# Kernel tuning notes

Hardware: AMD Instinct MI355X
Metric: run time of the kernel (lower is better)

The kernel has to match this reference:

```python
import jax, jax.numpy as jnp
import numpy as np

EPS = 1e-5

def conv1x1(x, w):
    # x: [B,C,T,D,H,W], w: [O,C] -> [B,O,T,D,H,W]
    return jnp.einsum('oc,bctdhw->botdhw', w, x)

def conv4d_3(x, w):
    # 3x3x3x3 4D conv, padding=1, stride=1, decomposed as 3 shifted 3D convs.
    # x: [B,C,T,D,H,W], w: [O,C,3,3,3,3]
    B, C, T, D, H, W = x.shape
    O = w.shape[0]
    xp = jnp.pad(x, ((0, 0), (0, 0), (1, 1), (1, 1), (1, 1), (1, 1)))
    out = None
    for k in range(3):  # small fixed loop over first kernel dim
        xk = xp[:, :, k:k + T]                      # [B,C,T,D+2,H+2,W+2]
        xk = xk.transpose(0, 2, 1, 3, 4, 5).reshape(B * T, C, D + 2, H + 2, W + 2)
        ok = jax.lax.conv_general_dilated(
            xk, w[:, :, k], window_strides=(1, 1, 1), padding='VALID',
            dimension_numbers=('NCDHW', 'OIDHW', 'NCDHW'))  # [B*T,O,D,H,W]
        out = ok if out is None else out + ok
    return out.reshape(B, T, O, D, H, W).transpose(0, 2, 1, 3, 4, 5)

def bn4d(x, g, b):
    # BatchNorm over (B, T, D, H, W) per channel (training-mode batch stats).
    axes = (0, 2, 3, 4, 5)
    m = jnp.mean(x, axis=axes, keepdims=True)
    v = jnp.mean(jnp.square(x - m), axis=axes, keepdims=True)
    sh = (1, -1, 1, 1, 1, 1)
    return (x - m) * jax.lax.rsqrt(v + EPS) * g.reshape(sh) + b.reshape(sh)

def setup_inputs() -> dict:
    key = jax.random.key(0)
    ks = jax.random.split(key, 4)
    B, C, T, D, H, W = 2, 256, 8, 16, 16, 16
    planes = 64
    return {
        'x': jax.random.normal(ks[0], (B, C, T, D, H, W), jnp.float32),
        'w1': jax.random.normal(ks[1], (planes, C), jnp.float32) * 0.05,
        'g1': jnp.ones((planes,), jnp.float32),
        'b1': jnp.zeros((planes,), jnp.float32),
        'w2': jax.random.normal(ks[2], (planes, planes, 3, 3, 3, 3), jnp.float32) * 0.05,
        'g2': jnp.ones((planes,), jnp.float32),
        'b2': jnp.zeros((planes,), jnp.float32),
        'w3': jax.random.normal(ks[3], (4 * planes, planes), jnp.float32) * 0.05,
        'g3': jnp.ones((4 * planes,), jnp.float32),
        'b3': jnp.zeros((4 * planes,), jnp.float32),
    }

def reference(x, w1, g1, b1, w2, g2, b2, w3, g3, b3):
    out = jax.nn.relu(bn4d(conv1x1(x, w1), g1, b1))
    out = jax.nn.relu(bn4d(conv4d_3(out, w2), g2, b2))
    out = bn4d(conv1x1(out, w3), g3, b3)
    return jax.nn.relu(out + x)
```

## Files before the change

### kernel.cpp

```cpp
#include <hip/hip_runtime.h>

#define S_TOT 32768

typedef unsigned short ushortT;
typedef __attribute__((ext_vector_type(8))) short short8;
typedef __attribute__((ext_vector_type(4))) float floatx4;

__device__ __forceinline__ ushortT f2bf(float f) {
    unsigned u = __float_as_uint(f);
    u = (u + 0x7fffu + ((u >> 16) & 1u)) >> 16;
    return (ushortT)u;
}
__device__ __forceinline__ float bf2f(ushortT h) {
    return __uint_as_float(((unsigned)h) << 16);
}
__device__ __forceinline__ uint32_t nrm2(uint32_t u, float a, float bs) {
    float lo = fmaxf(fmaf(a, bf2f((ushortT)(u & 0xffffu)), bs), 0.f);
    float hi = fmaxf(fmaf(a, bf2f((ushortT)(u >> 16)), bs), 0.f);
    return (uint32_t)f2bf(lo) | ((uint32_t)f2bf(hi) << 16);
}

#define NSTRIPE 8
#define STRIDE_ST 768

__global__ __launch_bounds__(256) void k_prep_w(const float* __restrict__ w1,
                                                const float* __restrict__ w2,
                                                const float* __restrict__ w3,
                                                ushortT* __restrict__ wb1,
                                                ushortT* __restrict__ wb2,
                                                ushortT* __restrict__ wb3,
                                                float* __restrict__ stats) {
    int idx = blockIdx.x * 256 + threadIdx.x;
    if (idx < 16384) {
        int e = idx;
        int j = e & 7, o = (e >> 3) & 63, q = (e >> 9) & 3, cc = e >> 11;
        int c = cc * 32 + q * 8 + j;
        wb1[e] = f2bf(w1[o * 256 + c]);
    } else if (idx < 16384 + 331776) {
        int e = idx - 16384;
        int j = e & 7, o = (e >> 3) & 63, cb = (e >> 9) & 7, tap = e >> 12;
        int c = cb * 8 + j;
        wb2[e] = f2bf(w2[((size_t)o * 64 + c) * 81 + tap]);
    } else if (idx < 16384 + 331776 + 16384) {
        int e = idx - 348160;
        int j = e & 7, o = (e >> 3) & 255, g = e >> 11;
        int ks = g >> 2, q = g & 3;
        int c = ks * 32 + q * 8 + j;
        wb3[e] = f2bf(w3[o * 64 + c]);
    } else if (idx < 364544 + NSTRIPE * STRIDE_ST) {
        stats[idx - 364544] = 0.f;
    }
}

__global__ __launch_bounds__(256) void k_conv1_mfma(const float* __restrict__ x,
                                                    const ushortT* __restrict__ wb1,
                                                    ushortT* __restrict__ y1bf,
                                                    float* __restrict__ stats) {
    __shared__ __align__(16) ushortT xb[128 * 40];

    int tid = threadIdx.x;
    int blk = blockIdx.x;
    int b  = blk >> 8;
    int n0 = (blk & 255) * 128;

    int lane = tid & 63;
    int wv   = tid >> 6;
    int m    = lane & 15;
    int q    = lane >> 4;

    int c_loc = tid & 31;
    int ng    = tid >> 5;

    floatx4 acc[8];
#pragma unroll
    for (int i = 0; i < 8; ++i) acc[i] = (floatx4){0.f, 0.f, 0.f, 0.f};

    for (int cc = 0; cc < 8; ++cc) {
        short8 afr = *(const short8*)(wb1 + (((cc * 4 + q) * 64) + wv * 16 + m) * 8);

        __syncthreads();
        {
            int c = cc * 32 + c_loc;
            const float* xp = x + ((size_t)(b * 256 + c)) * S_TOT + n0 + ng * 16;
#pragma unroll
            for (int k = 0; k < 4; ++k) {
                float4 v = *(const float4*)(xp + k * 4);
                int nb = ng * 16 + k * 4;
                xb[(nb + 0) * 40 + c_loc] = f2bf(v.x);
                xb[(nb + 1) * 40 + c_loc] = f2bf(v.y);
                xb[(nb + 2) * 40 + c_loc] = f2bf(v.z);
                xb[(nb + 3) * 40 + c_loc] = f2bf(v.w);
            }
        }
        __syncthreads();

#pragma unroll
        for (int pt = 0; pt < 8; ++pt) {
            short8 bfr = *(const short8*)(xb + (pt * 16 + m) * 40 + q * 8);
            acc[pt] = __builtin_amdgcn_mfma_f32_16x16x32_bf16(afr, bfr, acc[pt], 0, 0, 0);
        }
    }

#pragma unroll
    for (int pt = 0; pt < 8; ++pt) {
#pragma unroll
        for (int r = 0; r < 4; ++r) {
            int o = wv * 16 + q * 4 + r;
            y1bf[((size_t)(b * 64 + o)) * S_TOT + n0 + pt * 16 + m] = f2bf(acc[pt][r]);
        }
    }

    float ssum[4] = {0.f, 0.f, 0.f, 0.f}, ssq[4] = {0.f, 0.f, 0.f, 0.f};
#pragma unroll
    for (int pt = 0; pt < 8; ++pt)
#pragma unroll
        for (int r = 0; r < 4; ++r) {
            float v = acc[pt][r];
            ssum[r] += v;
            ssq[r]  += v * v;
        }
#pragma unroll
    for (int off = 1; off < 16; off <<= 1)
#pragma unroll
        for (int r = 0; r < 4; ++r) {
            ssum[r] += __shfl_xor(ssum[r], off);
            ssq[r]  += __shfl_xor(ssq[r], off);
        }
    if (m == 0) {
        float* st = stats + (blk & (NSTRIPE - 1)) * STRIDE_ST;
#pragma unroll
        for (int r = 0; r < 4; ++r) {
            int o = wv * 16 + q * 4 + r;
            atomicAdd(st + o, ssum[r]);
            atomicAdd(st + 64 + o, ssq[r]);
        }
    }
}

__global__ __launch_bounds__(256, 2) void k_conv2_mfma(
        const ushortT* __restrict__ y1bf,
        const ushortT* __restrict__ wb2,
        const float* __restrict__ g1,
        const float* __restrict__ b1,
        float* __restrict__ stats,
        ushortT* __restrict__ y2bf) {
    __shared__ __align__(16) ushortT xs[180 * 64];
    __shared__ float st2[128];

    int tid = threadIdx.x;
    int blk = blockIdx.x;
    int b  = blk >> 8;
    int t  = (blk >> 5) & 7;
    int d  = (blk >> 1) & 15;
    int h0 = (blk & 1) * 8;

    int lane = tid & 63;
    int wv   = tid >> 6;
    int m    = lane & 15;
    int q    = lane >> 4;
    int wp   = wv & 1;
    int wo   = wv >> 1;

    int c2      = tid & 31;
    int prbase  = tid >> 5;

    if (tid < 128) st2[tid] = 0.f;

    int c0 = 2 * c2, c1v = c0 + 1;
    float s0 = 0.f, q0 = 0.f, s1 = 0.f, q1 = 0.f;
#pragma unroll
    for (int p = 0; p < NSTRIPE; ++p) {
        const float* sp = stats + p * STRIDE_ST;
        s0 += sp[c0];  q0 += sp[64 + c0];
        s1 += sp[c1v]; q1 += sp[64 + c1v];
    }
    const float inv_n = 1.f / 65536.f;
    float mu0 = s0 * inv_n, var0 = q0 * inv_n - mu0 * mu0;
    float a0  = g1[c0] * rsqrtf(var0 + 1e-5f);
    float bb0 = b1[c0] - mu0 * a0;
    float mu1 = s1 * inv_n, var1 = q1 * inv_n - mu1 * mu1;
    float a1  = g1[c1v] * rsqrtf(var1 + 1e-5f);
    float bb1 = b1[c1v] - mu1 * a1;

    floatx4 acc[2][4];
#pragma unroll
    for (int i = 0; i < 2; ++i)
#pragma unroll
        for (int j = 0; j < 4; ++j) acc[i][j] = (floatx4){0.f, 0.f, 0.f, 0.f};

    const size_t cstride = 32768;
    uint32_t* xsd = (uint32_t*)xs;

    for (int ktd = 0; ktd < 9; ++ktd) {
        int kt = ktd / 3, kd = ktd - kt * 3;
        int tt = t + kt - 1;
        int dd = d + kd - 1;
        bool pv = (tt >= 0 && tt < 8 && dd >= 0 && dd < 16);
        if (!pv) continue;

        short8 afr[9][2][2];
#pragma unroll
        for (int khw = 0; khw < 9; ++khw) {
            int tap = ktd * 9 + khw;
#pragma unroll
            for (int ks = 0; ks < 2; ++ks)
#pragma unroll
                for (int ot = 0; ot < 2; ++ot) {
                    afr[khw][ks][ot] = *(const short8*)(wb2 +
                        (((size_t)(tap * 8 + ks * 4 + q)) * 64 + wo * 32 + ot * 16 + m) * 8);
                }
        }

        __syncthreads();

        for (int pr = prbase; pr < 10; pr += 8) {
            int hin = h0 + pr - 1;
            uint32_t pack[18];
            if (hin >= 0 && hin < 16) {
                const ushortT* p0 = y1bf +
                    (((size_t)(b * 64 + c0) * 8 + tt) * 16 + dd) * 256 + hin * 16;
                const ushortT* p1 = p0 + cstride;
                uint4 r0 = *(const uint4*)p0;
                uint4 r1 = *(const uint4*)(p0 + 8);
                uint4 s0v = *(const uint4*)p1;
                uint4 s1v = *(const uint4*)(p1 + 8);
                uint32_t ra[8] = {r0.x, r0.y, r0.z, r0.w, r1.x, r1.y, r1.z, r1.w};
                uint32_t sa[8] = {s0v.x, s0v.y, s0v.z, s0v.w, s1v.x, s1v.y, s1v.z, s1v.w};
#pragma unroll
                for (int k = 0; k < 8; ++k) {
                    ra[k] = nrm2(ra[k], a0, bb0);
                    sa[k] = nrm2(sa[k], a1, bb1);
                }
                pack[0] = 0; pack[17] = 0;
#pragma unroll
                for (int k = 0; k < 8; ++k) {
                    pack[1 + 2 * k] = (ra[k] & 0xffffu) | (sa[k] << 16);
                    pack[2 + 2 * k] = (ra[k] >> 16) | (sa[k] & 0xffff0000u);
                }
            } else {
#pragma unroll
                for (int k = 0; k < 18; ++k) pack[k] = 0;
            }
            int pb = pr * 18;
#pragma unroll
            for (int k = 0; k < 18; ++k) {
                int ppos = pb + k;
                xsd[ppos * 32 + ((((c2 >> 2) ^ (ppos & 7)) << 2) | (c2 & 3))] = pack[k];
            }
        }
        __syncthreads();

#pragma unroll
        for (int kh = 0; kh < 3; ++kh) {
#pragma unroll
            for (int kw = 0; kw < 3; ++kw) {
                int khw = kh * 3 + kw;
#pragma unroll
                for (int nt = 0; nt < 4; ++nt) {
                    int ppos = (wp * 4 + nt + kh) * 18 + m + kw;
                    int sw = (ppos & 7);
                    const ushortT* row = xs + ppos * 64;
                    short8 b0 = *(const short8*)(row + (((0 * 4 + q) ^ sw) << 3));
                    short8 b1f = *(const short8*)(row + (((1 * 4 + q) ^ sw) << 3));
                    acc[0][nt] = __builtin_amdgcn_mfma_f32_16x16x32_bf16(
                        afr[khw][0][0], b0, acc[0][nt], 0, 0, 0);
                    acc[1][nt] = __builtin_amdgcn_mfma_f32_16x16x32_bf16(
                        afr[khw][0][1], b0, acc[1][nt], 0, 0, 0);
                    acc[0][nt] = __builtin_amdgcn_mfma_f32_16x16x32_bf16(
                        afr[khw][1][0], b1f, acc[0][nt], 0, 0, 0);
                    acc[1][nt] = __builtin_amdgcn_mfma_f32_16x16x32_bf16(
                        afr[khw][1][1], b1f, acc[1][nt], 0, 0, 0);
                }
            }
        }
    }

#pragma unroll
    for (int ot = 0; ot < 2; ++ot) {
#pragma unroll
        for (int nt = 0; nt < 4; ++nt) {
#pragma unroll
            for (int r = 0; r < 4; ++r) {
                int o  = wo * 32 + ot * 16 + q * 4 + r;
                int hh = h0 + wp * 4 + nt;
                y2bf[(((size_t)(b * 64 + o) * 8 + t) * 16 + d) * 256 + hh * 16 + m] =
                    f2bf(acc[ot][nt][r]);
            }
        }
    }

    float ss[2][4], sqv[2][4];
#pragma unroll
    for (int ot = 0; ot < 2; ++ot)
#pragma unroll
        for (int r = 0; r < 4; ++r) {
            float s = 0.f, qv = 0.f;
#pragma unroll
            for (int nt = 0; nt < 4; ++nt) {
                float v = acc[ot][nt][r];
                s += v; qv += v * v;
            }
            ss[ot][r] = s; sqv[ot][r] = qv;
        }
#pragma unroll
    for (int off = 1; off < 16; off <<= 1)
#pragma unroll
        for (int ot = 0; ot < 2; ++ot)
#pragma unroll
            for (int r = 0; r < 4; ++r) {
                ss[ot][r]  += __shfl_xor(ss[ot][r], off);
                sqv[ot][r] += __shfl_xor(sqv[ot][r], off);
            }
    if (m == 0) {
#pragma unroll
        for (int ot = 0; ot < 2; ++ot)
#pragma unroll
            for (int r = 0; r < 4; ++r) {
                int o = wo * 32 + ot * 16 + q * 4 + r;
                atomicAdd(&st2[o], ss[ot][r]);
                atomicAdd(&st2[64 + o], sqv[ot][r]);
            }
    }
    __syncthreads();
    if (tid < 128)
        atomicAdd(stats + (blk & (NSTRIPE - 1)) * STRIDE_ST + 128 + tid, st2[tid]);
}

__global__ __launch_bounds__(256) void k_conv3_mfma(const ushortT* __restrict__ y2bf,
                                                    const ushortT* __restrict__ wb3,
                                                    const float* __restrict__ g2,
                                                    const float* __restrict__ b2,
                                                    float* __restrict__ stats,
                                                    float* __restrict__ y3) {
    __shared__ __align__(16) ushortT yb[64 * 72];

    int tid = threadIdx.x;
    int blk = blockIdx.x;
    int b  = blk >> 9;
    int n0 = (blk & 511) * 64;

    int lane = tid & 63;
    int wv   = tid >> 6;
    int m    = lane & 15;
    int q    = lane >> 4;

    const float inv_n = 1.f / 65536.f;
    for (int idx = tid; idx < 512; idx += 256) {
        int c = idx >> 3, k = idx & 7;
        float s = 0.f, qv = 0.f;
#pragma unroll
        for (int p = 0; p < NSTRIPE; ++p) {
            const float* sp = stats + p * STRIDE_ST;
            s += sp[128 + c]; qv += sp[192 + c];
        }
        float mu = s * inv_n, var = qv * inv_n - mu * mu;
        float a  = g2[c] * rsqrtf(var + 1e-5f);
        float bs = b2[c] - mu * a;
        uint4 v = *(const uint4*)(y2bf + ((size_t)(b * 64 + c)) * S_TOT + n0 + k * 8);
        uint32_t va[4] = {v.x, v.y, v.z, v.w};
#pragma unroll
        for (int p = 0; p < 4; ++p) {
            float lo = fmaxf(fmaf(a, bf2f((ushortT)(va[p] & 0xffffu)), bs), 0.f);
            float hi = fmaxf(fmaf(a, bf2f((ushortT)(va[p] >> 16)), bs), 0.f);
            yb[(k * 8 + 2 * p)     * 72 + c] = f2bf(lo);
            yb[(k * 8 + 2 * p + 1) * 72 + c] = f2bf(hi);
        }
    }
    __syncthreads();

    floatx4 acc[4][4];
#pragma unroll
    for (int i = 0; i < 4; ++i)
#pragma unroll
        for (int j = 0; j < 4; ++j) acc[i][j] = (floatx4){0.f, 0.f, 0.f, 0.f};

#pragma unroll
    for (int ks = 0; ks < 2; ++ks) {
        short8 afr[4];
#pragma unroll
        for (int ot = 0; ot < 4; ++ot)
            afr[ot] = *(const short8*)(wb3 +
                (((ks * 4 + q) * 256) + wv * 64 + ot * 16 + m) * 8);
#pragma unroll
        for (int pt = 0; pt < 4; ++pt) {
            short8 bfr = *(const short8*)(yb + (pt * 16 + m) * 72 + ks * 32 + q * 8);
#pragma unroll
            for (int ot = 0; ot < 4; ++ot)
                acc[ot][pt] = __builtin_amdgcn_mfma_f32_16x16x32_bf16(
                    afr[ot], bfr, acc[ot][pt], 0, 0, 0);
        }
    }

#pragma unroll
    for (int ot = 0; ot < 4; ++ot) {
#pragma unroll
        for (int pt = 0; pt < 4; ++pt) {
#pragma unroll
            for (int r = 0; r < 4; ++r) {
                int o = wv * 64 + ot * 16 + q * 4 + r;
                y3[((size_t)(b * 256 + o)) * S_TOT + n0 + pt * 16 + m] = acc[ot][pt][r];
            }
        }
    }

    float ssum[4][4], ssq[4][4];
#pragma unroll
    for (int ot = 0; ot < 4; ++ot)
#pragma unroll
        for (int r = 0; r < 4; ++r) {
            float s = 0.f, qv = 0.f;
#pragma unroll
            for (int pt = 0; pt < 4; ++pt) {
                float v = acc[ot][pt][r];
                s += v; qv += v * v;
            }
            ssum[ot][r] = s; ssq[ot][r] = qv;
        }
#pragma unroll
    for (int off = 1; off < 16; off <<= 1)
#pragma unroll
        for (int ot = 0; ot < 4; ++ot)
#pragma unroll
            for (int r = 0; r < 4; ++r) {
                ssum[ot][r] += __shfl_xor(ssum[ot][r], off);
                ssq[ot][r]  += __shfl_xor(ssq[ot][r], off);
            }
    if (m == 0) {
        float* st = stats + (blk & (NSTRIPE - 1)) * STRIDE_ST;
#pragma unroll
        for (int ot = 0; ot < 4; ++ot)
#pragma unroll
            for (int r = 0; r < 4; ++r) {
                int o = wv * 64 + ot * 16 + q * 4 + r;
                atomicAdd(st + 256 + o, ssum[ot][r]);
                atomicAdd(st + 512 + o, ssq[ot][r]);
            }
    }
}

__global__ __launch_bounds__(256) void k_final(const float* __restrict__ x,
                                               const float* __restrict__ stats,
                                               const float* __restrict__ g,
                                               const float* __restrict__ bb,
                                               float* __restrict__ out) {
    size_t i = ((size_t)blockIdx.x * 256 + threadIdx.x) * 4;
    int o = (int)((blockIdx.x >> 5) & 255);
    float s = 0.f, qv = 0.f;
#pragma unroll
    for (int p = 0; p < NSTRIPE; ++p) {
        s  += stats[p * STRIDE_ST + 256 + o];
        qv += stats[p * STRIDE_ST + 512 + o];
    }
    const float n = 65536.f;
    float mean = s / n;
    float var  = qv / n - mean * mean;
    float a  = g[o] * rsqrtf(var + 1e-5f);
    float bs = bb[o] - mean * a;
    float4 y  = *(float4*)(out + i);
    float4 xv = *(const float4*)(x + i);
    float4 r;
    r.x = fmaxf(a * y.x + bs + xv.x, 0.f);
    r.y = fmaxf(a * y.y + bs + xv.y, 0.f);
    r.z = fmaxf(a * y.z + bs + xv.z, 0.f);
    r.w = fmaxf(a * y.w + bs + xv.w, 0.f);
    *(float4*)(out + i) = r;
}

extern "C" void kernel_launch(void* const* d_in, const int* in_sizes, int n_in,
                              void* d_out, int out_size, void* d_ws, size_t ws_size,
                              hipStream_t stream) {
    const float* x  = (const float*)d_in[0];
    const float* w1 = (const float*)d_in[1];
    const float* g1 = (const float*)d_in[2];
    const float* b1 = (const float*)d_in[3];
    const float* w2 = (const float*)d_in[4];
    const float* g2 = (const float*)d_in[5];
    const float* b2 = (const float*)d_in[6];
    const float* w3 = (const float*)d_in[7];
    const float* g3 = (const float*)d_in[8];
    const float* b3 = (const float*)d_in[9];

    char* ws = (char*)d_ws;
    ushortT* y1bf = (ushortT*)(ws);
    ushortT* y2bf = (ushortT*)(ws + 8388608);
    ushortT* wb1  = (ushortT*)(ws + 16777216);
    ushortT* wb2  = (ushortT*)(ws + 16809984);
    ushortT* wb3  = (ushortT*)(ws + 17473536);
    float*   stats = (float*)(ws + 17506304);
    float* y3 = (float*)d_out;

    k_prep_w     <<<1448,  256, 0, stream>>>(w1, w2, w3, wb1, wb2, wb3, stats);
    k_conv1_mfma <<<512,   256, 0, stream>>>(x, wb1, y1bf, stats);
    k_conv2_mfma <<<512,   256, 0, stream>>>(y1bf, wb2, g1, b1, stats, y2bf);
    k_conv3_mfma <<<1024,  256, 0, stream>>>(y2bf, wb3, g2, b2, stats, y3);
    k_final      <<<16384, 256, 0, stream>>>(x, stats, g3, b3, y3);
}
```

Baseline: 262.3 us.

## Prefetch next conv2 input slice into registers and precompute BN coefficients

The conv2 kernel now loads the next valid (t,d) input slice from global memory into registers while the MFMA loop for the current slice runs. This hides global load latency behind compute. Block indices are remapped so consecutive blocks spread across the (b,t,d) space, which changes L2/XCD locality. BN scale and shift for layers 1 and 2 are computed once by a small single-block kernel instead of by every block, at the cost of two extra launches and more live registers in conv2, which could reduce occupancy.

```diff
diff --git a/kernel.cpp b/kernel.cpp
--- a/kernel.cpp
+++ b/kernel.cpp
@@ -52,6 +52,26 @@
     }
 }
 
+__global__ __launch_bounds__(256) void k_coef(const float* __restrict__ stats,
+                                              int off, int nch,
+                                              const float* __restrict__ g,
+                                              const float* __restrict__ bb,
+                                              float* __restrict__ coef) {
+    int c = threadIdx.x;
+    if (c >= nch) return;
+    float s = 0.f, qv = 0.f;
+#pragma unroll
+    for (int p = 0; p < NSTRIPE; ++p) {
+        s  += stats[p * STRIDE_ST + off + c];
+        qv += stats[p * STRIDE_ST + off + nch + c];
+    }
+    const float inv_n = 1.f / 65536.f;
+    float mu = s * inv_n, var = qv * inv_n - mu * mu;
+    float a  = g[c] * rsqrtf(var + 1e-5f);
+    coef[2 * c]     = a;
+    coef[2 * c + 1] = bb[c] - mu * a;
+}
+
 __global__ __launch_bounds__(256) void k_conv1_mfma(const float* __restrict__ x,
                                                     const ushortT* __restrict__ wb1,
                                                     ushortT* __restrict__ y1bf,
@@ -140,15 +160,15 @@
 __global__ __launch_bounds__(256, 2) void k_conv2_mfma(
         const ushortT* __restrict__ y1bf,
         const ushortT* __restrict__ wb2,
-        const float* __restrict__ g1,
-        const float* __restrict__ b1,
+        const float* __restrict__ coef1,
         float* __restrict__ stats,
         ushortT* __restrict__ y2bf) {
     __shared__ __align__(16) ushortT xs[180 * 64];
     __shared__ float st2[128];
 
     int tid = threadIdx.x;
-    int blk = blockIdx.x;
+    int hw  = blockIdx.x;
+    int blk = (hw & 7) * 64 + (hw >> 3);
     int b  = blk >> 8;
     int t  = (blk >> 5) & 7;
     int d  = (blk >> 1) & 15;
@@ -163,24 +183,14 @@
 
     int c2      = tid & 31;
     int prbase  = tid >> 5;
+    bool hasB   = (prbase < 2);
 
     if (tid < 128) st2[tid] = 0.f;
 
     int c0 = 2 * c2, c1v = c0 + 1;
-    float s0 = 0.f, q0 = 0.f, s1 = 0.f, q1 = 0.f;
-#pragma unroll
-    for (int p = 0; p < NSTRIPE; ++p) {
-        const float* sp = stats + p * STRIDE_ST;
-        s0 += sp[c0];  q0 += sp[64 + c0];
-        s1 += sp[c1v]; q1 += sp[64 + c1v];
-    }
-    const float inv_n = 1.f / 65536.f;
-    float mu0 = s0 * inv_n, var0 = q0 * inv_n - mu0 * mu0;
-    float a0  = g1[c0] * rsqrtf(var0 + 1e-5f);
-    float bb0 = b1[c0] - mu0 * a0;
-    float mu1 = s1 * inv_n, var1 = q1 * inv_n - mu1 * mu1;
-    float a1  = g1[c1v] * rsqrtf(var1 + 1e-5f);
-    float bb1 = b1[c1v] - mu1 * a1;
+    float2 cA = *(const float2*)(coef1 + 2 * c0);
+    float2 cB = *(const float2*)(coef1 + 2 * c1v);
+    float a0 = cA.x, bb0 = cA.y, a1 = cB.x, bb1 = cB.y;
 
     floatx4 acc[2][4];
 #pragma unroll
@@ -191,17 +201,45 @@
     const size_t cstride = 32768;
     uint32_t* xsd = (uint32_t*)xs;
 
-    for (int ktd = 0; ktd < 9; ++ktd) {
-        int kt = ktd / 3, kd = ktd - kt * 3;
-        int tt = t + kt - 1;
-        int dd = d + kd - 1;
-        bool pv = (tt >= 0 && tt < 8 && dd >= 0 && dd < 16);
-        if (!pv) continue;
+    uint4 Ar0, Ar1, As0, As1, Br0, Br1, Bs0, Bs1;
+    bool okA = false, okB = false;
+
+    int kcur = 0, tt = 0, dd = 0;
+    for (;; ++kcur) {
+        int kt = kcur / 3, kd = kcur - kt * 3;
+        tt = t + kt - 1; dd = d + kd - 1;
+        if (tt >= 0 && tt < 8 && dd >= 0 && dd < 16) break;
+    }
+    {
+        const ushortT* bp = y1bf + (((size_t)(b * 64 + c0) * 8 + tt) * 16 + dd) * 256;
+        int hinA = h0 + prbase - 1;
+        okA = (hinA >= 0) && (hinA < 16);
+        if (okA) {
+            const ushortT* p = bp + hinA * 16;
+            Ar0 = *(const uint4*)p;             Ar1 = *(const uint4*)(p + 8);
+            As0 = *(const uint4*)(p + cstride); As1 = *(const uint4*)(p + cstride + 8);
+        }
+        int hinB = h0 + prbase + 7;
+        okB = hasB && (hinB < 16);
+        if (okB) {
+            const ushortT* p = bp + hinB * 16;
+            Br0 = *(const uint4*)p;             Br1 = *(const uint4*)(p + 8);
+            Bs0 = *(const uint4*)(p + cstride); Bs1 = *(const uint4*)(p + cstride + 8);
+        }
+    }
+
+    while (kcur < 9) {
+        int knext = kcur + 1, tt2 = 0, dd2 = 0;
+        for (; knext < 9; ++knext) {
+            int kt = knext / 3, kd = knext - kt * 3;
+            tt2 = t + kt - 1; dd2 = d + kd - 1;
+            if (tt2 >= 0 && tt2 < 8 && dd2 >= 0 && dd2 < 16) break;
+        }
 
         short8 afr[9][2][2];
 #pragma unroll
         for (int khw = 0; khw < 9; ++khw) {
-            int tap = ktd * 9 + khw;
+            int tap = kcur * 9 + khw;
 #pragma unroll
             for (int ks = 0; ks < 2; ++ks)
 #pragma unroll
@@ -213,19 +251,11 @@
 
         __syncthreads();
 
-        for (int pr = prbase; pr < 10; pr += 8) {
-            int hin = h0 + pr - 1;
+        {
             uint32_t pack[18];
-            if (hin >= 0 && hin < 16) {
-                const ushortT* p0 = y1bf +
-                    (((size_t)(b * 64 + c0) * 8 + tt) * 16 + dd) * 256 + hin * 16;
-                const ushortT* p1 = p0 + cstride;
-                uint4 r0 = *(const uint4*)p0;
-                uint4 r1 = *(const uint4*)(p0 + 8);
-                uint4 s0v = *(const uint4*)p1;
-                uint4 s1v = *(const uint4*)(p1 + 8);
-                uint32_t ra[8] = {r0.x, r0.y, r0.z, r0.w, r1.x, r1.y, r1.z, r1.w};
-                uint32_t sa[8] = {s0v.x, s0v.y, s0v.z, s0v.w, s1v.x, s1v.y, s1v.z, s1v.w};
+            if (okA) {
+                uint32_t ra[8] = {Ar0.x, Ar0.y, Ar0.z, Ar0.w, Ar1.x, Ar1.y, Ar1.z, Ar1.w};
+                uint32_t sa[8] = {As0.x, As0.y, As0.z, As0.w, As1.x, As1.y, As1.z, As1.w};
 #pragma unroll
                 for (int k = 0; k < 8; ++k) {
                     ra[k] = nrm2(ra[k], a0, bb0);
@@ -241,14 +271,60 @@
 #pragma unroll
                 for (int k = 0; k < 18; ++k) pack[k] = 0;
             }
-            int pb = pr * 18;
+            int pb = prbase * 18;
 #pragma unroll
             for (int k = 0; k < 18; ++k) {
                 int ppos = pb + k;
                 xsd[ppos * 32 + ((((c2 >> 2) ^ (ppos & 7)) << 2) | (c2 & 3))] = pack[k];
             }
         }
+        if (hasB) {
+            uint32_t pack[18];
+            if (okB) {
+                uint32_t ra[8] = {Br0.x, Br0.y, Br0.z, Br0.w, Br1.x, Br1.y, Br1.z, Br1.w};
+                uint32_t sa[8] = {Bs0.x, Bs0.y, Bs0.z, Bs0.w, Bs1.x, Bs1.y, Bs1.z, Bs1.w};
+#pragma unroll
+                for (int k = 0; k < 8; ++k) {
+                    ra[k] = nrm2(ra[k], a0, bb0);
+                    sa[k] = nrm2(sa[k], a1, bb1);
+                }
+                pack[0] = 0; pack[17] = 0;
+#pragma unroll
+                for (int k = 0; k < 8; ++k) {
+                    pack[1 + 2 * k] = (ra[k] & 0xffffu) | (sa[k] << 16);
+                    pack[2 + 2 * k] = (ra[k] >> 16) | (sa[k] & 0xffff0000u);
+                }
+            } else {
+#pragma unroll
+                for (int k = 0; k < 18; ++k) pack[k] = 0;
+            }
+            int pb = (prbase + 8) * 18;
+#pragma unroll
+            for (int k = 0; k < 18; ++k) {
+                int ppos = pb + k;
+                xsd[ppos * 32 + ((((c2 >> 2) ^ (ppos & 7)) << 2) | (c2 & 3))] = pack[k];
+            }
+        }
+
         __syncthreads();
+
+        if (knext < 9) {
+            const ushortT* bp = y1bf + (((size_t)(b * 64 + c0) * 8 + tt2) * 16 + dd2) * 256;
+            int hinA = h0 + prbase - 1;
+            okA = (hinA >= 0) && (hinA < 16);
+            if (okA) {
+                const ushortT* p = bp + hinA * 16;
+                Ar0 = *(const uint4*)p;             Ar1 = *(const uint4*)(p + 8);
+                As0 = *(const uint4*)(p + cstride); As1 = *(const uint4*)(p + cstride + 8);
+            }
+            int hinB = h0 + prbase + 7;
+            okB = hasB && (hinB < 16);
+            if (okB) {
+                const ushortT* p = bp + hinB * 16;
+                Br0 = *(const uint4*)p;             Br1 = *(const uint4*)(p + 8);
+                Bs0 = *(const uint4*)(p + cstride); Bs1 = *(const uint4*)(p + cstride + 8);
+            }
+        }
 
 #pragma unroll
         for (int kh = 0; kh < 3; ++kh) {
@@ -273,6 +349,8 @@
                 }
             }
         }
+
+        kcur = knext; tt = tt2; dd = dd2;
     }
 
 #pragma unroll
@@ -328,8 +406,7 @@
 
 __global__ __launch_bounds__(256) void k_conv3_mfma(const ushortT* __restrict__ y2bf,
                                                     const ushortT* __restrict__ wb3,
-                                                    const float* __restrict__ g2,
-                                                    const float* __restrict__ b2,
+                                                    const float* __restrict__ coef2,
                                                     float* __restrict__ stats,
                                                     float* __restrict__ y3) {
     __shared__ __align__(16) ushortT yb[64 * 72];
@@ -344,18 +421,10 @@
     int m    = lane & 15;
     int q    = lane >> 4;
 
-    const float inv_n = 1.f / 65536.f;
     for (int idx = tid; idx < 512; idx += 256) {
         int c = idx >> 3, k = idx & 7;
-        float s = 0.f, qv = 0.f;
-#pragma unroll
-        for (int p = 0; p < NSTRIPE; ++p) {
-            const float* sp = stats + p * STRIDE_ST;
-            s += sp[128 + c]; qv += sp[192 + c];
-        }
-        float mu = s * inv_n, var = qv * inv_n - mu * mu;
-        float a  = g2[c] * rsqrtf(var + 1e-5f);
-        float bs = b2[c] - mu * a;
+        float2 cc2 = *(const float2*)(coef2 + 2 * c);
+        float a = cc2.x, bs = cc2.y;
         uint4 v = *(const uint4*)(y2bf + ((size_t)(b * 64 + c)) * S_TOT + n0 + k * 8);
         uint32_t va[4] = {v.x, v.y, v.z, v.w};
 #pragma unroll
@@ -487,11 +556,15 @@
     ushortT* wb2  = (ushortT*)(ws + 16809984);
     ushortT* wb3  = (ushortT*)(ws + 17473536);
     float*   stats = (float*)(ws + 17506304);
+    float*   coef1 = (float*)(ws + 17530880);
+    float*   coef2 = (float*)(ws + 17531392);
     float* y3 = (float*)d_out;
 
     k_prep_w     <<<1448,  256, 0, stream>>>(w1, w2, w3, wb1, wb2, wb3, stats);
     k_conv1_mfma <<<512,   256, 0, stream>>>(x, wb1, y1bf, stats);
-    k_conv2_mfma <<<512,   256, 0, stream>>>(y1bf, wb2, g1, b1, stats, y2bf);
-    k_conv3_mfma <<<1024,  256, 0, stream>>>(y2bf, wb3, g2, b2, stats, y3);
+    k_coef       <<<1,     256, 0, stream>>>(stats, 0, 64, g1, b1, coef1);
+    k_conv2_mfma <<<512,   256, 0, stream>>>(y1bf, wb2, coef1, stats, y2bf);
+    k_coef       <<<1,     256, 0, stream>>>(stats, 128, 64, g2, b2, coef2);
+    k_conv3_mfma <<<1024,  256, 0, stream>>>(y2bf, wb3, coef2, stats, y3);
     k_final      <<<16384, 256, 0, stream>>>(x, stats, g3, b3, y3);
 }
```

New measurement: 378.0 us. 44.2% more time.
